# Optimization experiments

Measured on AMD Instinct MI355X. Metric: run time of the kernel, lower is better.

## Reference

```python
import jax, jax.numpy as jnp
import numpy as np

INPUT_DIM = 1024
CODEBOOK_DIM = 128
CODEBOOK_SIZE = 8192
B, N = 8, 4096


def setup_inputs() -> dict:
    key = jax.random.key(0)
    k1, k2, k3 = jax.random.split(key, 3)
    x = jax.random.normal(k1, (B, N, INPUT_DIM), dtype=jnp.float32)
    # xavier_normal_: std = sqrt(2 / (fan_in + fan_out))
    xavier_std = float(np.sqrt(2.0 / (INPUT_DIM + CODEBOOK_DIM)))
    random_projection = jax.random.normal(k2, (INPUT_DIM, CODEBOOK_DIM), dtype=jnp.float32) * xavier_std
    codebook = jax.random.normal(k3, (CODEBOOK_SIZE, CODEBOOK_DIM), dtype=jnp.float32)
    return {"x": x, "random_projection": random_projection, "codebook": codebook}


def reference(x, random_projection, codebook):
    # random projection: [B, N, D] @ [D, E] -> [B, N, E]
    proj = jnp.einsum("bnd,de->bne", x, random_projection)
    b, n, e = proj.shape
    flat = proj.reshape(b * n, e)  # [BN, E]
    eps = 1e-12  # matches torch F.normalize default eps
    nx = flat / jnp.maximum(jnp.linalg.norm(flat, axis=1, keepdims=True), eps)
    ncb = codebook / jnp.maximum(jnp.linalg.norm(codebook, axis=1, keepdims=True), eps)
    # squared euclidean distances [K, BN]; argmin of d^2 == argmin of cdist
    d2 = (
        jnp.sum(ncb * ncb, axis=1)[:, None]
        + jnp.sum(nx * nx, axis=1)[None, :]
        - 2.0 * (ncb @ nx.T)
    )
    nearest = jnp.argmin(d2, axis=0)  # [BN]
    return nearest.reshape(b, n).astype(jnp.int32)
```

## Files before the change

### kernel.cpp

```cpp
#include <hip/hip_runtime.h>
#include <math.h>
#include <float.h>
#include <limits.h>

#define BN      32768
#define D_IN    1024
#define E_DIM   128
#define CB_N    8192

typedef _Float16 f16x8 __attribute__((ext_vector_type(8)));
typedef _Float16 f16x4 __attribute__((ext_vector_type(4)));
typedef float    f32x4 __attribute__((ext_vector_type(4)));


__global__ __launch_bounds__(256) void pack_kernel(
    const float* __restrict__ cb, const float* __restrict__ rp,
    _Float16* __restrict__ ph, _Float16* __restrict__ pl,
    _Float16* __restrict__ rph, _Float16* __restrict__ rpl) {
    const int t = threadIdx.x;
    if (blockIdx.x < 512) {
        __shared__ float L[16][129];
        const int g = blockIdx.x;
        const int c = t >> 4, p = t & 15;
        const float4 v0 = *(const float4*)&cb[(size_t)(g * 16 + c) * E_DIM + p * 8];
        const float4 v1 = *(const float4*)&cb[(size_t)(g * 16 + c) * E_DIM + p * 8 + 4];
        float ss = v0.x * v0.x + v0.y * v0.y + v0.z * v0.z + v0.w * v0.w
                 + v1.x * v1.x + v1.y * v1.y + v1.z * v1.z + v1.w * v1.w;
#pragma unroll
        for (int m = 1; m < 16; m <<= 1) ss += __shfl_xor(ss, m);
        const float inv = 256.0f / fmaxf(sqrtf(ss), 1e-12f);

        L[c][p * 8 + 0] = v0.x * inv; L[c][p * 8 + 1] = v0.y * inv;
        L[c][p * 8 + 2] = v0.z * inv; L[c][p * 8 + 3] = v0.w * inv;
        L[c][p * 8 + 4] = v1.x * inv; L[c][p * 8 + 5] = v1.y * inv;
        L[c][p * 8 + 6] = v1.z * inv; L[c][p * 8 + 7] = v1.w * inv;
        __syncthreads();

        const int kb = t >> 6, lane = t & 63;
        const int quad = (lane >> 4), col = lane & 15;
        f16x8 h, l;
#pragma unroll
        for (int j = 0; j < 8; ++j) {
            const float v = L[col][kb * 32 + quad * 8 + j];
            const _Float16 hv = (_Float16)v;
            h[j] = hv;
            l[j] = (_Float16)(v - (float)hv);
        }
        const size_t off = ((size_t)(g * 4 + kb) * 64 + lane) * 8;
        *(f16x8*)&ph[off] = h;
        *(f16x8*)&pl[off] = l;
    } else {
        const int w = t >> 6, lane = t & 63;
        const int b = (blockIdx.x - 512) * 4 + w;
        const int kb = b >> 3, nt = b & 7;
        const int quad = lane >> 4, col = lane & 15;
        f16x8 h, l;
#pragma unroll
        for (int j = 0; j < 8; ++j) {
            const float v = rp[(size_t)(kb * 32 + quad * 8 + j) * E_DIM + nt * 16 + col] * 64.0f;
            const _Float16 hv = (_Float16)v;
            h[j] = hv;
            l[j] = (_Float16)(v - (float)hv);
        }
        const size_t off = ((size_t)b * 64 + lane) * 8;
        *(f16x8*)&rph[off] = h;
        *(f16x8*)&rpl[off] = l;
    }
}

#define PAD_ROW 40
#define PPITCH  132

__global__ __launch_bounds__(256, 2) void fused_kernel(
    const float* __restrict__ x,
    const _Float16* __restrict__ rph, const _Float16* __restrict__ rpl,
    const _Float16* __restrict__ ph, const _Float16* __restrict__ pl,
    int* __restrict__ out) {
    __shared__ _Float16 Ah[64 * PAD_ROW];
    __shared__ _Float16 Al[64 * PAD_ROW];
    __shared__ float    P[64 * PPITCH];
    __shared__ float    ls[4][64];
    __shared__ int      li[4][64];

    const int tid  = threadIdx.x;
    const int lane = tid & 63;
    const int w    = tid >> 6;
    const int quad = lane >> 4, col = lane & 15;
    const int qb   = blockIdx.x * 64;

    const int srow = tid >> 3;
    const int skc  = (tid & 7) * 4;

    f32x4 acc[4][2];
#pragma unroll
    for (int mt = 0; mt < 4; ++mt)
#pragma unroll
        for (int h = 0; h < 2; ++h) acc[mt][h] = (f32x4){0.f, 0.f, 0.f, 0.f};

    float4 pre[2];
#pragma unroll
    for (int i = 0; i < 2; ++i)
        pre[i] = *(const float4*)&x[(size_t)(qb + srow + 32 * i) * D_IN + skc];

    for (int kb = 0; kb < 32; ++kb) {
#pragma unroll
        for (int i = 0; i < 2; ++i) {
            const float vv[4] = {pre[i].x, pre[i].y, pre[i].z, pre[i].w};
            f16x4 h4, l4;
#pragma unroll
            for (int j = 0; j < 4; ++j) {
                const float v = vv[j] * 512.0f;
                const _Float16 hv = (_Float16)v;
                h4[j] = hv;
                l4[j] = (_Float16)(v - (float)hv);
            }
            const int base = (srow + 32 * i) * PAD_ROW + skc;
            *(f16x4*)&Ah[base] = h4;
            *(f16x4*)&Al[base] = l4;
        }
        __syncthreads();

        if (kb + 1 < 32) {
#pragma unroll
            for (int i = 0; i < 2; ++i)
                pre[i] = *(const float4*)&x[(size_t)(qb + srow + 32 * i) * D_IN + (kb + 1) * 32 + skc];
        }

        f16x8 bh1[2], bl1[2];
#pragma unroll
        for (int h = 0; h < 2; ++h) {
            const int nt = w * 2 + h;
            const size_t off = ((size_t)(kb * 8 + nt) * 64 + lane) * 8;
            bh1[h] = *(const f16x8*)&rph[off];
            bl1[h] = *(const f16x8*)&rpl[off];
        }

        f16x8 ah1[4], al1[4];
#pragma unroll
        for (int mt = 0; mt < 4; ++mt) {
            const int base = (mt * 16 + col) * PAD_ROW + quad * 8;
            ah1[mt] = *(const f16x8*)&Ah[base];
            al1[mt] = *(const f16x8*)&Al[base];
        }

#pragma unroll
        for (int mt = 0; mt < 4; ++mt)
#pragma unroll
            for (int h = 0; h < 2; ++h)
                acc[mt][h] = __builtin_amdgcn_mfma_f32_16x16x32_f16(ah1[mt], bh1[h], acc[mt][h], 0, 0, 0);
#pragma unroll
        for (int mt = 0; mt < 4; ++mt)
#pragma unroll
            for (int h = 0; h < 2; ++h)
                acc[mt][h] = __builtin_amdgcn_mfma_f32_16x16x32_f16(ah1[mt], bl1[h], acc[mt][h], 0, 0, 0);
#pragma unroll
        for (int mt = 0; mt < 4; ++mt)
#pragma unroll
            for (int h = 0; h < 2; ++h)
                acc[mt][h] = __builtin_amdgcn_mfma_f32_16x16x32_f16(al1[mt], bh1[h], acc[mt][h], 0, 0, 0);

        __syncthreads();
    }

#pragma unroll
    for (int mt = 0; mt < 4; ++mt)
#pragma unroll
        for (int h = 0; h < 2; ++h)
#pragma unroll
            for (int r = 0; r < 4; ++r)
                P[(mt * 16 + quad * 4 + r) * PPITCH + w * 32 + h * 16 + col]
                    = acc[mt][h][r] * (1.0f / 2048.0f);

    const int g0 = w * 128;
    f16x8 bh[2][4], bl[2][4];
#pragma unroll
    for (int kb = 0; kb < 4; ++kb) {
        const size_t off = ((size_t)(g0 * 4 + kb) * 64 + lane) * 8;
        bh[0][kb] = *(const f16x8*)&ph[off];
        bl[0][kb] = *(const f16x8*)&pl[off];
    }
    __syncthreads();

    f16x8 ahF[4][4], alF[4][4];
#pragma unroll
    for (int mt = 0; mt < 4; ++mt)
#pragma unroll
        for (int kbb = 0; kbb < 4; ++kbb) {
            const int base = (mt * 16 + col) * PPITCH + kbb * 32 + quad * 8;
            const float4 v0 = *(const float4*)&P[base];
            const float4 v1 = *(const float4*)&P[base + 4];
            const float vv[8] = {v0.x, v0.y, v0.z, v0.w, v1.x, v1.y, v1.z, v1.w};
            f16x8 hh, ll;
#pragma unroll
            for (int j = 0; j < 8; ++j) {
                const _Float16 hv = (_Float16)vv[j];
                hh[j] = hv;
                ll[j] = (_Float16)(vv[j] - (float)hv);
            }
            ahF[mt][kbb] = hh;
            alF[mt][kbb] = ll;
        }

    float bs[16];
    int   bi[16];
#pragma unroll
    for (int s = 0; s < 16; ++s) { bs[s] = -FLT_MAX; bi[s] = 0; }

#pragma unroll 2
    for (int t = 0; t < 128; ++t) {
        const int cur = t & 1, nxt = cur ^ 1;
        if (t + 1 < 128) {
            const int gn = g0 + t + 1;
#pragma unroll
            for (int kb = 0; kb < 4; ++kb) {
                const size_t off = ((size_t)(gn * 4 + kb) * 64 + lane) * 8;
                bh[nxt][kb] = *(const f16x8*)&ph[off];
                bl[nxt][kb] = *(const f16x8*)&pl[off];
            }
        }

        f32x4 sacc[4];
#pragma unroll
        for (int mt = 0; mt < 4; ++mt) sacc[mt] = (f32x4){0.f, 0.f, 0.f, 0.f};

#pragma unroll
        for (int kb = 0; kb < 4; ++kb)
#pragma unroll
            for (int mt = 0; mt < 4; ++mt)
                sacc[mt] = __builtin_amdgcn_mfma_f32_16x16x32_f16(ahF[mt][kb], bh[cur][kb], sacc[mt], 0, 0, 0);
#pragma unroll
        for (int kb = 0; kb < 4; ++kb)
#pragma unroll
            for (int mt = 0; mt < 4; ++mt)
                sacc[mt] = __builtin_amdgcn_mfma_f32_16x16x32_f16(ahF[mt][kb], bl[cur][kb], sacc[mt], 0, 0, 0);
#pragma unroll
        for (int kb = 0; kb < 4; ++kb)
#pragma unroll
            for (int mt = 0; mt < 4; ++mt)
                sacc[mt] = __builtin_amdgcn_mfma_f32_16x16x32_f16(alF[mt][kb], bh[cur][kb], sacc[mt], 0, 0, 0);

        const int code = (g0 + t) * 16 + col;
#pragma unroll
        for (int mt = 0; mt < 4; ++mt)
#pragma unroll
            for (int r = 0; r < 4; ++r) {
                const float v = sacc[mt][r];
                const int s = mt * 4 + r;
                if (v > bs[s]) { bs[s] = v; bi[s] = code; }
            }
    }

#pragma unroll
    for (int s = 0; s < 16; ++s) {
#pragma unroll
        for (int m = 1; m < 16; m <<= 1) {
            const float os = __shfl_xor(bs[s], m);
            const int   oi = __shfl_xor(bi[s], m);
            if (os > bs[s] || (os == bs[s] && oi < bi[s])) { bs[s] = os; bi[s] = oi; }
        }
    }

    if (col == 0) {
#pragma unroll
        for (int mt = 0; mt < 4; ++mt)
#pragma unroll
            for (int r = 0; r < 4; ++r) {
                ls[w][mt * 16 + quad * 4 + r] = bs[mt * 4 + r];
                li[w][mt * 16 + quad * 4 + r] = bi[mt * 4 + r];
            }
    }
    __syncthreads();

    if (tid < 64) {
        float s = ls[0][tid];
        int   i = li[0][tid];
#pragma unroll
        for (int ww = 1; ww < 4; ++ww) {
            const float os = ls[ww][tid];
            if (os > s) { s = os; i = li[ww][tid]; }
        }
        out[qb + tid] = i;
    }
}

extern "C" void kernel_launch(void* const* d_in, const int* in_sizes, int n_in,
                              void* d_out, int out_size, void* d_ws, size_t ws_size,
                              hipStream_t stream) {
    const float* x  = (const float*)d_in[0];
    const float* rp = (const float*)d_in[1];
    const float* cb = (const float*)d_in[2];
    int* out = (int*)d_out;

    _Float16* ph  = (_Float16*)d_ws;
    _Float16* pl  = ph  + (size_t)CB_N * E_DIM;
    _Float16* rph = pl  + (size_t)CB_N * E_DIM;
    _Float16* rpl = rph + (size_t)D_IN * E_DIM;

    pack_kernel<<<576, 256, 0, stream>>>(cb, rp, ph, pl, rph, rpl);
    fused_kernel<<<BN / 64, 256, 0, stream>>>(x, rph, rpl, ph, pl, out);
}
```

Baseline: 399.9 us.

## Halve the row tile to 32, alias shared memory, and target three blocks per CU

```diff
diff --git a/kernel.cpp b/kernel.cpp
--- a/kernel.cpp
+++ b/kernel.cpp
@@ -71,41 +71,38 @@
 #define PAD_ROW 40
 #define PPITCH  132
 
-__global__ __launch_bounds__(256, 2) void fused_kernel(
+__global__ __launch_bounds__(256, 3) void fused_kernel(
     const float* __restrict__ x,
     const _Float16* __restrict__ rph, const _Float16* __restrict__ rpl,
     const _Float16* __restrict__ ph, const _Float16* __restrict__ pl,
     int* __restrict__ out) {
-    __shared__ _Float16 Ah[64 * PAD_ROW];
-    __shared__ _Float16 Al[64 * PAD_ROW];
-    __shared__ float    P[64 * PPITCH];
-    __shared__ float    ls[4][64];
-    __shared__ int      li[4][64];
+    __shared__ __align__(16) unsigned char smem[17408];
+    _Float16* Ah = (_Float16*)smem;
+    _Float16* Al = (_Float16*)(smem + 2560);
+    float*    P  = (float*)smem;
+    float*    ls = (float*)smem;
+    int*      li = (int*)(smem + 512);
 
     const int tid  = threadIdx.x;
     const int lane = tid & 63;
     const int w    = tid >> 6;
     const int quad = lane >> 4, col = lane & 15;
-    const int qb   = blockIdx.x * 64;
+    const int qb   = blockIdx.x * 32;
 
     const int srow = tid >> 3;
     const int skc  = (tid & 7) * 4;
 
-    f32x4 acc[4][2];
-#pragma unroll
-    for (int mt = 0; mt < 4; ++mt)
+    f32x4 acc[2][2];
+#pragma unroll
+    for (int mt = 0; mt < 2; ++mt)
 #pragma unroll
         for (int h = 0; h < 2; ++h) acc[mt][h] = (f32x4){0.f, 0.f, 0.f, 0.f};
 
-    float4 pre[2];
-#pragma unroll
-    for (int i = 0; i < 2; ++i)
-        pre[i] = *(const float4*)&x[(size_t)(qb + srow + 32 * i) * D_IN + skc];
+    float4 pre = *(const float4*)&x[(size_t)(qb + srow) * D_IN + skc];
 
     for (int kb = 0; kb < 32; ++kb) {
-#pragma unroll
-        for (int i = 0; i < 2; ++i) {
-            const float vv[4] = {pre[i].x, pre[i].y, pre[i].z, pre[i].w};
+        {
+            const float vv[4] = {pre.x, pre.y, pre.z, pre.w};
             f16x4 h4, l4;
 #pragma unroll
             for (int j = 0; j < 4; ++j) {
@@ -114,17 +111,14 @@
                 h4[j] = hv;
                 l4[j] = (_Float16)(v - (float)hv);
             }
-            const int base = (srow + 32 * i) * PAD_ROW + skc;
+            const int base = srow * PAD_ROW + skc;
             *(f16x4*)&Ah[base] = h4;
             *(f16x4*)&Al[base] = l4;
         }
         __syncthreads();
 
-        if (kb + 1 < 32) {
-#pragma unroll
-            for (int i = 0; i < 2; ++i)
-                pre[i] = *(const float4*)&x[(size_t)(qb + srow + 32 * i) * D_IN + (kb + 1) * 32 + skc];
-        }
+        if (kb + 1 < 32)
+            pre = *(const float4*)&x[(size_t)(qb + srow) * D_IN + (kb + 1) * 32 + skc];
 
         f16x8 bh1[2], bl1[2];
 #pragma unroll
@@ -135,26 +129,26 @@
             bl1[h] = *(const f16x8*)&rpl[off];
         }
 
-        f16x8 ah1[4], al1[4];
-#pragma unroll
-        for (int mt = 0; mt < 4; ++mt) {
+        f16x8 ah1[2], al1[2];
+#pragma unroll
+        for (int mt = 0; mt < 2; ++mt) {
             const int base = (mt * 16 + col) * PAD_ROW + quad * 8;
             ah1[mt] = *(const f16x8*)&Ah[base];
             al1[mt] = *(const f16x8*)&Al[base];
         }
 
 #pragma unroll
-        for (int mt = 0; mt < 4; ++mt)
+        for (int mt = 0; mt < 2; ++mt)
 #pragma unroll
             for (int h = 0; h < 2; ++h)
                 acc[mt][h] = __builtin_amdgcn_mfma_f32_16x16x32_f16(ah1[mt], bh1[h], acc[mt][h], 0, 0, 0);
 #pragma unroll
-        for (int mt = 0; mt < 4; ++mt)
+        for (int mt = 0; mt < 2; ++mt)
 #pragma unroll
             for (int h = 0; h < 2; ++h)
                 acc[mt][h] = __builtin_amdgcn_mfma_f32_16x16x32_f16(ah1[mt], bl1[h], acc[mt][h], 0, 0, 0);
 #pragma unroll
-        for (int mt = 0; mt < 4; ++mt)
+        for (int mt = 0; mt < 2; ++mt)
 #pragma unroll
             for (int h = 0; h < 2; ++h)
                 acc[mt][h] = __builtin_amdgcn_mfma_f32_16x16x32_f16(al1[mt], bh1[h], acc[mt][h], 0, 0, 0);
@@ -163,7 +157,7 @@
     }
 
 #pragma unroll
-    for (int mt = 0; mt < 4; ++mt)
+    for (int mt = 0; mt < 2; ++mt)
 #pragma unroll
         for (int h = 0; h < 2; ++h)
 #pragma unroll
@@ -181,12 +175,12 @@
     }
     __syncthreads();
 
-    f16x8 ahF[4][4], alF[4][4];
-#pragma unroll
-    for (int mt = 0; mt < 4; ++mt)
+    f16x8 ahF[2][4], alF[2][4];
+#pragma unroll
+    for (int mt2 = 0; mt2 < 2; ++mt2)
 #pragma unroll
         for (int kbb = 0; kbb < 4; ++kbb) {
-            const int base = (mt * 16 + col) * PPITCH + kbb * 32 + quad * 8;
+            const int base = (mt2 * 16 + col) * PPITCH + kbb * 32 + quad * 8;
             const float4 v0 = *(const float4*)&P[base];
             const float4 v1 = *(const float4*)&P[base + 4];
             const float vv[8] = {v0.x, v0.y, v0.z, v0.w, v1.x, v1.y, v1.z, v1.w};
@@ -197,14 +191,14 @@
                 hh[j] = hv;
                 ll[j] = (_Float16)(vv[j] - (float)hv);
             }
-            ahF[mt][kbb] = hh;
-            alF[mt][kbb] = ll;
-        }
-
-    float bs[16];
-    int   bi[16];
-#pragma unroll
-    for (int s = 0; s < 16; ++s) { bs[s] = -FLT_MAX; bi[s] = 0; }
+            ahF[mt2][kbb] = hh;
+            alF[mt2][kbb] = ll;
+        }
+
+    float bs[8];
+    int   bi[8];
+#pragma unroll
+    for (int s = 0; s < 8; ++s) { bs[s] = -FLT_MAX; bi[s] = 0; }
 
 #pragma unroll 2
     for (int t = 0; t < 128; ++t) {
@@ -218,40 +212,36 @@
                 bl[nxt][kb] = *(const f16x8*)&pl[off];
             }
         }
-
-        f32x4 sacc[4];
-#pragma unroll
-        for (int mt = 0; mt < 4; ++mt) sacc[mt] = (f32x4){0.f, 0.f, 0.f, 0.f};
-
-#pragma unroll
-        for (int kb = 0; kb < 4; ++kb)
-#pragma unroll
-            for (int mt = 0; mt < 4; ++mt)
-                sacc[mt] = __builtin_amdgcn_mfma_f32_16x16x32_f16(ahF[mt][kb], bh[cur][kb], sacc[mt], 0, 0, 0);
-#pragma unroll
-        for (int kb = 0; kb < 4; ++kb)
-#pragma unroll
-            for (int mt = 0; mt < 4; ++mt)
-                sacc[mt] = __builtin_amdgcn_mfma_f32_16x16x32_f16(ahF[mt][kb], bl[cur][kb], sacc[mt], 0, 0, 0);
-#pragma unroll
-        for (int kb = 0; kb < 4; ++kb)
-#pragma unroll
-            for (int mt = 0; mt < 4; ++mt)
-                sacc[mt] = __builtin_amdgcn_mfma_f32_16x16x32_f16(alF[mt][kb], bh[cur][kb], sacc[mt], 0, 0, 0);
+        __builtin_amdgcn_sched_barrier(0);
+
+        f32x4 s0 = (f32x4){0.f, 0.f, 0.f, 0.f};
+        f32x4 s1 = (f32x4){0.f, 0.f, 0.f, 0.f};
+#pragma unroll
+        for (int kb = 0; kb < 4; ++kb) {
+            s0 = __builtin_amdgcn_mfma_f32_16x16x32_f16(ahF[0][kb], bh[cur][kb], s0, 0, 0, 0);
+            s1 = __builtin_amdgcn_mfma_f32_16x16x32_f16(ahF[1][kb], bh[cur][kb], s1, 0, 0, 0);
+        }
+#pragma unroll
+        for (int kb = 0; kb < 4; ++kb) {
+            s0 = __builtin_amdgcn_mfma_f32_16x16x32_f16(ahF[0][kb], bl[cur][kb], s0, 0, 0, 0);
+            s1 = __builtin_amdgcn_mfma_f32_16x16x32_f16(ahF[1][kb], bl[cur][kb], s1, 0, 0, 0);
+        }
+#pragma unroll
+        for (int kb = 0; kb < 4; ++kb) {
+            s0 = __builtin_amdgcn_mfma_f32_16x16x32_f16(alF[0][kb], bh[cur][kb], s0, 0, 0, 0);
+            s1 = __builtin_amdgcn_mfma_f32_16x16x32_f16(alF[1][kb], bh[cur][kb], s1, 0, 0, 0);
+        }
 
         const int code = (g0 + t) * 16 + col;
 #pragma unroll
-        for (int mt = 0; mt < 4; ++mt)
-#pragma unroll
-            for (int r = 0; r < 4; ++r) {
-                const float v = sacc[mt][r];
-                const int s = mt * 4 + r;
-                if (v > bs[s]) { bs[s] = v; bi[s] = code; }
-            }
-    }
-
-#pragma unroll
-    for (int s = 0; s < 16; ++s) {
+        for (int r = 0; r < 4; ++r) {
+            if (s0[r] > bs[r])     { bs[r] = s0[r];     bi[r] = code; }
+            if (s1[r] > bs[4 + r]) { bs[4 + r] = s1[r]; bi[4 + r] = code; }
+        }
+    }
+
+#pragma unroll
+    for (int s = 0; s < 8; ++s) {
 #pragma unroll
         for (int m = 1; m < 16; m <<= 1) {
             const float os = __shfl_xor(bs[s], m);
@@ -262,22 +252,22 @@
 
     if (col == 0) {
 #pragma unroll
-        for (int mt = 0; mt < 4; ++mt)
+        for (int mt2 = 0; mt2 < 2; ++mt2)
 #pragma unroll
             for (int r = 0; r < 4; ++r) {
-                ls[w][mt * 16 + quad * 4 + r] = bs[mt * 4 + r];
-                li[w][mt * 16 + quad * 4 + r] = bi[mt * 4 + r];
+                ls[w * 32 + mt2 * 16 + quad * 4 + r] = bs[mt2 * 4 + r];
+                li[w * 32 + mt2 * 16 + quad * 4 + r] = bi[mt2 * 4 + r];
             }
     }
     __syncthreads();
 
-    if (tid < 64) {
-        float s = ls[0][tid];
-        int   i = li[0][tid];
+    if (tid < 32) {
+        float s = ls[tid];
+        int   i = li[tid];
 #pragma unroll
         for (int ww = 1; ww < 4; ++ww) {
-            const float os = ls[ww][tid];
-            if (os > s) { s = os; i = li[ww][tid]; }
+            const float os = ls[ww * 32 + tid];
+            if (os > s) { s = os; i = li[ww * 32 + tid]; }
         }
         out[qb + tid] = i;
     }
@@ -297,5 +287,5 @@
     _Float16* rpl = rph + (size_t)D_IN * E_DIM;
 
     pack_kernel<<<576, 256, 0, stream>>>(cb, rp, ph, pl, rph, rpl);
-    fused_kernel<<<BN / 64, 256, 0, stream>>>(x, rph, rpl, ph, pl, out);
+    fused_kernel<<<BN / 32, 256, 0, stream>>>(x, rph, rpl, ph, pl, out);
 }
```

Result: slower. 447.5 us (+11.9%).
